# Kernel tuning notes

Hardware: AMD Instinct MI355X
Metric: run time of the kernel (lower is better)

The kernel has to match this reference:

```python
import jax, jax.numpy as jnp
import numpy as np

WINDOW_SIZE = 256  # module init arg


def setup_inputs() -> dict:
    key = jax.random.key(0)
    # (B, H, T, D) population matrix; nonnegative values keep denom = mean + 0.5 well away from 0
    pop = jax.random.uniform(key, (2, 16, 2048, 64), dtype=jnp.float32)
    return {"population_matrix": pop}


def reference(population_matrix):
    B, H, T, D = population_matrix.shape
    dt = population_matrix.dtype
    ones = jnp.ones((T, T), dtype=dt)
    mask = jnp.tril(ones)  # causal (T, T)
    if WINDOW_SIZE is not None:
        window_mask = jnp.tril(ones, 0) - jnp.tril(ones, -WINDOW_SIZE)
        mask = mask * window_mask
    # number of active (unmasked) positions per query row, clamped to >= 1
    counts = jnp.maximum(mask.sum(axis=1), 1.0)  # (T,)
    # gene_means[b,h,i,d] = sum_j mask[i,j] * pop[b,h,j,d] / counts[i]  -- a GEMM
    gene_means = jnp.einsum('ij,bhjd->bhid', mask, population_matrix) / counts[None, None, :, None]
    denom = gene_means + 0.5  # (B,H,T,D)
    sum_inv_denom = jnp.sum(1.0 / denom, axis=-1, keepdims=True)  # (B,H,T,1)
    gene_fitness = 1.0 / (denom * sum_inv_denom)  # (B,H,T,D)
    # org_fitness[b,h,i,j] = mask[i,j] * sum_d pop[b,h,j,d] * gene_fitness[b,h,i,d]
    org_fitness = jnp.einsum('bhid,bhjd->bhij', gene_fitness, population_matrix) * mask
    row_sums = jnp.maximum(org_fitness.sum(axis=-1, keepdims=True), 1e-10)
    return org_fitness / row_sums
```

## Files before the change

kernel.cpp:

```cpp
#include <hip/hip_runtime.h>
#include <cstdint>

#define T_  2048
#define D_  64
#define BH_ 32
#define W_  256
#define GP  72

typedef float f32x4 __attribute__((ext_vector_type(4)));
using bf16x8 = __attribute__((ext_vector_type(8))) short;

__device__ inline unsigned short f2bf(float x) {
  unsigned u = __float_as_uint(x);
  u = (u + 0x7fffu + ((u >> 16) & 1u)) >> 16;
  return (unsigned short)u;
}

__device__ inline bf16x8 cvt8(const f32x4 lo, const f32x4 hi) {
  bf16x8 r;
  r[0] = (short)f2bf(lo.x); r[1] = (short)f2bf(lo.y);
  r[2] = (short)f2bf(lo.z); r[3] = (short)f2bf(lo.w);
  r[4] = (short)f2bf(hi.x); r[5] = (short)f2bf(hi.y);
  r[6] = (short)f2bf(hi.z); r[7] = (short)f2bf(hi.w);
  return r;
}

__global__ __launch_bounds__(256, 2) void fused_strip(const float* __restrict__ pop,
                                                      float* __restrict__ out) {
  __shared__ unsigned short Gs[128 * GP];
  const int unit = blockIdx.x;
  const int i0   = (unit & 15) * 128;
  const int bh   = unit >> 4;
  const int tid  = threadIdx.x;
  const int lane = tid & 63, wv = tid >> 6;
  const int l15 = lane & 15, l4 = lane >> 4;
  const float* Pb = pop + (size_t)bh * T_ * D_;
  float*       Ob = out + (size_t)bh * T_ * T_;
  const int ib0 = i0 + wv * 32;

  {
    const int d = lane;
    const float* P = Pb + d;

    int s0 = ib0 - (W_ - 1); if (s0 < 0) s0 = 0;
    const int jend = ib0 + 1;
    float p0=0.f,p1=0.f,p2=0.f,p3=0.f,p4=0.f,p5=0.f,p6=0.f,p7=0.f;
    int j = s0;
    for (; j + 8 <= jend; j += 8) {
      p0 += P[(size_t)(j+0)*D_]; p1 += P[(size_t)(j+1)*D_];
      p2 += P[(size_t)(j+2)*D_]; p3 += P[(size_t)(j+3)*D_];
      p4 += P[(size_t)(j+4)*D_]; p5 += P[(size_t)(j+5)*D_];
      p6 += P[(size_t)(j+6)*D_]; p7 += P[(size_t)(j+7)*D_];
    }
    for (; j < jend; ++j) p0 += P[(size_t)j*D_];
    const float isum0 = ((p0+p1)+(p2+p3)) + ((p4+p5)+(p6+p7));

    float arrv[32], depv[32];
    arrv[0] = 0.f; depv[0] = 0.f;
    #pragma unroll
    for (int r = 1; r < 32; ++r) arrv[r] = P[(size_t)(ib0 + r) * D_];
    #pragma unroll
    for (int r = 1; r < 32; ++r) {
      const int jd = ib0 + r - W_;
      depv[r] = (jd >= 0) ? P[(size_t)jd * D_] : 0.f;
    }

    float rinv[32];
    float run = isum0;
    #pragma unroll
    for (int r = 0; r < 32; ++r) {
      run += arrv[r] - depv[r];
      const int i = ib0 + r;
      const float cnt = (i + 1 < W_) ? (float)(i + 1) : (float)W_;
      rinv[r] = 1.0f / (run / cnt + 0.5f);
    }

    float sv[32];
    #pragma unroll
    for (int r = 0; r < 32; ++r) sv[r] = rinv[r];
    #pragma unroll
    for (int m = 32; m >= 1; m >>= 1) {
      #pragma unroll
      for (int r = 0; r < 32; ++r) sv[r] += __shfl_xor(sv[r], m);
    }

    #pragma unroll
    for (int r = 0; r < 32; ++r) {
      const int i = ib0 + r;
      const float cnt = (i + 1 < W_) ? (float)(i + 1) : (float)W_;
      float rowsum = cnt * (64.0f / sv[r] - 0.5f);
      rowsum = fmaxf(rowsum, 1e-10f);
      Gs[(wv * 32 + r) * GP + d] = f2bf(rinv[r] / (rowsum * sv[r]));
    }
  }
  __syncthreads();

  const bf16x8 g00 = *reinterpret_cast<const bf16x8*>(&Gs[(wv*32      + l15) * GP      + l4*8]);
  const bf16x8 g01 = *reinterpret_cast<const bf16x8*>(&Gs[(wv*32      + l15) * GP + 32 + l4*8]);
  const bf16x8 g10 = *reinterpret_cast<const bf16x8*>(&Gs[(wv*32 + 16 + l15) * GP      + l4*8]);
  const bf16x8 g11 = *reinterpret_cast<const bf16x8*>(&Gs[(wv*32 + 16 + l15) * GP + 32 + l4*8]);

  for (int jt = 0; jt < 24; ++jt) {
    const int jb = i0 - 256 + jt * 16;
    if (jb < 0) continue;
    const float* prow = &Pb[(size_t)(jb + l15) * D_];
    const f32x4 q0 = *reinterpret_cast<const f32x4*>(prow + l4*8);
    const f32x4 q1 = *reinterpret_cast<const f32x4*>(prow + l4*8 + 4);
    const f32x4 q2 = *reinterpret_cast<const f32x4*>(prow + 32 + l4*8);
    const f32x4 q3 = *reinterpret_cast<const f32x4*>(prow + 32 + l4*8 + 4);
    const bf16x8 p0 = cvt8(q0, q1);
    const bf16x8 p1 = cvt8(q2, q3);

    f32x4 c0 = {0.f, 0.f, 0.f, 0.f};
    f32x4 c1 = {0.f, 0.f, 0.f, 0.f};
    c0 = __builtin_amdgcn_mfma_f32_16x16x32_bf16(p0, g00, c0, 0, 0, 0);
    c0 = __builtin_amdgcn_mfma_f32_16x16x32_bf16(p1, g01, c0, 0, 0, 0);
    c1 = __builtin_amdgcn_mfma_f32_16x16x32_bf16(p0, g10, c1, 0, 0, 0);
    c1 = __builtin_amdgcn_mfma_f32_16x16x32_bf16(p1, g11, c1, 0, 0, 0);

    const int jq = jb + l4 * 4;
    {
      const int i = ib0 + l15;
      f32x4 v;
      #pragma unroll
      for (int r = 0; r < 4; ++r)
        v[r] = ((unsigned)(i - (jq + r)) < 256u) ? c0[r] : 0.f;
      *reinterpret_cast<f32x4*>(&Ob[(size_t)i * T_ + jq]) = v;
    }
    {
      const int i = ib0 + 16 + l15;
      f32x4 v;
      #pragma unroll
      for (int r = 0; r < 4; ++r)
        v[r] = ((unsigned)(i - (jq + r)) < 256u) ? c1[r] : 0.f;
      *reinterpret_cast<f32x4*>(&Ob[(size_t)i * T_ + jq]) = v;
    }
  }

  {
    int Lz = i0 - 256; if (Lz < 0) Lz = 0;
    const int L4n = Lz >> 2;
    const int R   = i0 + 128;
    const int W4r = (T_ - R) >> 2;
    const f32x4 z4 = {0.f, 0.f, 0.f, 0.f};
    for (int r = 0; r < 32; ++r) {
      float* orow = Ob + (size_t)(ib0 + r) * T_;
      f32x4* oL = reinterpret_cast<f32x4*>(orow);
      for (int c = lane; c < L4n; c += 64)
        __builtin_nontemporal_store(z4, &oL[c]);
      f32x4* oR = reinterpret_cast<f32x4*>(orow + R);
      for (int c = lane; c < W4r; c += 64)
        __builtin_nontemporal_store(z4, &oR[c]);
    }
  }
}

extern "C" void kernel_launch(void* const* d_in, const int* in_sizes, int n_in,
                              void* d_out, int out_size, void* d_ws, size_t ws_size,
                              hipStream_t stream) {
  const float* pop = (const float*)d_in[0];
  float* out = (float*)d_out;
  dim3 blk(256);
  hipLaunchKernelGGL(fused_strip, dim3(16 * BH_), blk, 0, stream, pop, out);
}
```

Measured before the change: 132.5 us.

## Specialize extra waves for zero-fill and drop block barrier

Doubles the block to 512 threads. Waves 4-7 only write the zero regions of each row strip with nontemporal stores, while waves 0-3 compute the gene-fitness tile and run the MFMA band writes, so the two streams of stores can overlap. The per-row fitness computation is split into four chunks of 8 rows to shrink register arrays, which should help occupancy at the larger block size. The __syncthreads is removed because each wave only reads the shared-memory rows it wrote itself. Since the kernel is dominated by output store bandwidth, the overlap gain may be small, and the work split between the two wave groups is uneven.

```diff
diff --git a/kernel.cpp b/kernel.cpp
--- a/kernel.cpp
+++ b/kernel.cpp
@@ -25,7 +25,7 @@
   return r;
 }
 
-__global__ __launch_bounds__(256, 2) void fused_strip(const float* __restrict__ pop,
+__global__ __launch_bounds__(512, 2) void fused_strip(const float* __restrict__ pop,
                                                       float* __restrict__ out) {
   __shared__ unsigned short Gs[128 * GP];
   const int unit = blockIdx.x;
@@ -33,9 +33,29 @@
   const int bh   = unit >> 4;
   const int tid  = threadIdx.x;
   const int lane = tid & 63, wv = tid >> 6;
-  const int l15 = lane & 15, l4 = lane >> 4;
   const float* Pb = pop + (size_t)bh * T_ * D_;
   float*       Ob = out + (size_t)bh * T_ * T_;
+
+  if (wv >= 4) {
+    const int rb = i0 + (wv - 4) * 32;
+    int Lz = i0 - 256; if (Lz < 0) Lz = 0;
+    const int L4n = Lz >> 2;
+    const int R   = i0 + 128;
+    const int W4r = (T_ - R) >> 2;
+    const f32x4 z4 = {0.f, 0.f, 0.f, 0.f};
+    for (int r = 0; r < 32; ++r) {
+      float* orow = Ob + (size_t)(rb + r) * T_;
+      f32x4* oL = reinterpret_cast<f32x4*>(orow);
+      for (int c = lane; c < L4n; c += 64)
+        __builtin_nontemporal_store(z4, &oL[c]);
+      f32x4* oR = reinterpret_cast<f32x4*>(orow + R);
+      for (int c = lane; c < W4r; c += 64)
+        __builtin_nontemporal_store(z4, &oR[c]);
+    }
+    return;
+  }
+
+  const int l15 = lane & 15, l4 = lane >> 4;
   const int ib0 = i0 + wv * 32;
 
   {
@@ -53,47 +73,42 @@
       p6 += P[(size_t)(j+6)*D_]; p7 += P[(size_t)(j+7)*D_];
     }
     for (; j < jend; ++j) p0 += P[(size_t)j*D_];
-    const float isum0 = ((p0+p1)+(p2+p3)) + ((p4+p5)+(p6+p7));
-
-    float arrv[32], depv[32];
-    arrv[0] = 0.f; depv[0] = 0.f;
-    #pragma unroll
-    for (int r = 1; r < 32; ++r) arrv[r] = P[(size_t)(ib0 + r) * D_];
-    #pragma unroll
-    for (int r = 1; r < 32; ++r) {
-      const int jd = ib0 + r - W_;
-      depv[r] = (jd >= 0) ? P[(size_t)jd * D_] : 0.f;
-    }
-
-    float rinv[32];
-    float run = isum0;
-    #pragma unroll
-    for (int r = 0; r < 32; ++r) {
-      run += arrv[r] - depv[r];
-      const int i = ib0 + r;
-      const float cnt = (i + 1 < W_) ? (float)(i + 1) : (float)W_;
-      rinv[r] = 1.0f / (run / cnt + 0.5f);
-    }
-
-    float sv[32];
-    #pragma unroll
-    for (int r = 0; r < 32; ++r) sv[r] = rinv[r];
-    #pragma unroll
-    for (int m = 32; m >= 1; m >>= 1) {
-      #pragma unroll
-      for (int r = 0; r < 32; ++r) sv[r] += __shfl_xor(sv[r], m);
-    }
+    float run = ((p0+p1)+(p2+p3)) + ((p4+p5)+(p6+p7));
 
     #pragma unroll
-    for (int r = 0; r < 32; ++r) {
-      const int i = ib0 + r;
-      const float cnt = (i + 1 < W_) ? (float)(i + 1) : (float)W_;
-      float rowsum = cnt * (64.0f / sv[r] - 0.5f);
-      rowsum = fmaxf(rowsum, 1e-10f);
-      Gs[(wv * 32 + r) * GP + d] = f2bf(rinv[r] / (rowsum * sv[r]));
+    for (int c = 0; c < 4; ++c) {
+      float av[8], dv[8];
+      #pragma unroll
+      for (int k = 0; k < 8; ++k) {
+        const int r = c * 8 + k;
+        av[k] = (r == 0) ? 0.f : P[(size_t)(ib0 + r) * D_];
+        const int jd = ib0 + r - W_;
+        dv[k] = (r == 0 || jd < 0) ? 0.f : P[(size_t)jd * D_];
+      }
+      float rinv[8], sv[8];
+      #pragma unroll
+      for (int k = 0; k < 8; ++k) {
+        run += av[k] - dv[k];
+        const int i = ib0 + c * 8 + k;
+        const float cnt = (i + 1 < W_) ? (float)(i + 1) : (float)W_;
+        rinv[k] = 1.0f / (run / cnt + 0.5f);
+        sv[k] = rinv[k];
+      }
+      #pragma unroll
+      for (int m = 32; m >= 1; m >>= 1) {
+        #pragma unroll
+        for (int k = 0; k < 8; ++k) sv[k] += __shfl_xor(sv[k], m);
+      }
+      #pragma unroll
+      for (int k = 0; k < 8; ++k) {
+        const int i = ib0 + c * 8 + k;
+        const float cnt = (i + 1 < W_) ? (float)(i + 1) : (float)W_;
+        float rowsum = cnt * (64.0f / sv[k] - 0.5f);
+        rowsum = fmaxf(rowsum, 1e-10f);
+        Gs[(wv * 32 + c * 8 + k) * GP + d] = f2bf(rinv[k] / (rowsum * sv[k]));
+      }
     }
   }
-  __syncthreads();
 
   const bf16x8 g00 = *reinterpret_cast<const bf16x8*>(&Gs[(wv*32      + l15) * GP      + l4*8]);
   const bf16x8 g01 = *reinterpret_cast<const bf16x8*>(&Gs[(wv*32      + l15) * GP + 32 + l4*8]);
@@ -136,23 +151,6 @@
       *reinterpret_cast<f32x4*>(&Ob[(size_t)i * T_ + jq]) = v;
     }
   }
-
-  {
-    int Lz = i0 - 256; if (Lz < 0) Lz = 0;
-    const int L4n = Lz >> 2;
-    const int R   = i0 + 128;
-    const int W4r = (T_ - R) >> 2;
-    const f32x4 z4 = {0.f, 0.f, 0.f, 0.f};
-    for (int r = 0; r < 32; ++r) {
-      float* orow = Ob + (size_t)(ib0 + r) * T_;
-      f32x4* oL = reinterpret_cast<f32x4*>(orow);
-      for (int c = lane; c < L4n; c += 64)
-        __builtin_nontemporal_store(z4, &oL[c]);
-      f32x4* oR = reinterpret_cast<f32x4*>(orow + R);
-      for (int c = lane; c < W4r; c += 64)
-        __builtin_nontemporal_store(z4, &oR[c]);
-    }
-  }
 }
 
 extern "C" void kernel_launch(void* const* d_in, const int* in_sizes, int n_in,
@@ -160,6 +158,6 @@
                               hipStream_t stream) {
   const float* pop = (const float*)d_in[0];
   float* out = (float*)d_out;
-  dim3 blk(256);
+  dim3 blk(512);
   hipLaunchKernelGGL(fused_strip, dim3(16 * BH_), blk, 0, stream, pop, out);
 }
```

Measured after the change: 118.4 us. 1.12x faster.
